# Kernel optimization log

Measured on AMD Instinct MI355X. Metric: run time of the kernel, lower is better.

## Reference

```python
import jax, jax.numpy as jnp
import numpy as np

T, B, H, V, L = 512, 8, 256, 32000, 3
THRESH = 1.0

# Heaviside spike with ATan surrogate gradient (snntorch default, alpha=2)
@jax.custom_vjp
def spike(u):
    return (u > 0).astype(u.dtype)

def _spike_fwd(u):
    return (u > 0).astype(u.dtype), u

def _spike_bwd(u, g):
    return (g / (1.0 + (jnp.pi * u) ** 2),)

spike.defvjp(_spike_fwd, _spike_bwd)


def leaky_scan(cur, beta):
    """mem[t] = beta * mem[t-1] + cur[t]; cur: (T,B,H), beta: (H,). No reset -> associative."""
    def step(mem, c):
        mem = beta * mem + c
        return mem, mem
    _, mems = jax.lax.scan(step, jnp.zeros(cur.shape[1:], cur.dtype), cur)
    return mems  # (T,B,H)


def setup_inputs() -> dict:
    key = jax.random.key(0)
    ks = jax.random.split(key, 10)
    s = 1.0 / np.sqrt(H)
    return {
        "tokens": jax.random.randint(ks[0], (T, B), 0, V),
        "token_emb": jax.random.normal(ks[1], (V, H), dtype=jnp.float32) * 0.02,
        "pos_emb": jax.random.normal(ks[2], (T, H), dtype=jnp.float32) * 0.02,
        "Wq": jax.random.normal(ks[3], (L, H, H), dtype=jnp.float32) * s,
        "bq": jnp.zeros((L, H), dtype=jnp.float32),
        "beta": jax.random.uniform(ks[4], (L, H), minval=0.5, maxval=0.95),
        "Wfc": jax.random.normal(ks[5], (L, H, H), dtype=jnp.float32) * s,
        "bfc": jnp.zeros((L, H), dtype=jnp.float32),
        "Wout": jax.random.normal(ks[6], (H, V), dtype=jnp.float32) * s,
        "bout": jnp.zeros((V,), dtype=jnp.float32),
    }


def reference(tokens, token_emb, pos_emb, Wq, bq, beta, Wfc, bfc, Wout, bout):
    # embed: (T,B,H) + broadcast positional (T,1,H)
    h = token_emb[tokens] + pos_emb[:, None, :]
    for l in range(L):  # small fixed layer count
        cur = jnp.einsum('tbh,hd->tbd', h, Wq[l]) + bq[l]   # q-projection
        mem = leaky_scan(cur, beta[l])                       # leaky integrate, no reset
        spk = spike(mem - THRESH)                            # heaviside spikes
        h = jax.nn.relu(jnp.einsum('tbh,hd->tbd', spk, Wfc[l]) + bfc[l])
    logits = jnp.einsum('tbh,hv->tbv', h, Wout) + bout       # (T,B,V)
    return logits
```

## Files before the change

### kernel.cpp

```cpp
#include <hip/hip_runtime.h>
#include <hip/hip_bf16.h>
#include <cstddef>

constexpr int T_ = 512;
constexpr int B_ = 8;
constexpr int H_ = 256;
constexpr int V_ = 32000;
constexpr int L_ = 3;
constexpr int M_ = T_ * B_;

typedef __attribute__((ext_vector_type(8))) short short8;
typedef __attribute__((ext_vector_type(4))) float floatx4;

__device__ __forceinline__ unsigned short f2bf(float f) {
    unsigned u = __float_as_uint(f);
    u += 0x7fffu + ((u >> 16) & 1u);
    return (unsigned short)(u >> 16);
}

__device__ __forceinline__ void gl_lds16(const void* g, void* l) {
    __builtin_amdgcn_global_load_lds((__attribute__((address_space(1))) void*)g,
                                     (__attribute__((address_space(3))) void*)l,
                                     16, 0, 0);
}

__global__ __launch_bounds__(256) void embed_kernel(
    const int* __restrict__ tokens, const float* __restrict__ temb,
    const float* __restrict__ pemb, unsigned short* __restrict__ hb)
{
    const int idx = blockIdx.x * 256 + threadIdx.x;
    const int h4 = idx & (H_ / 4 - 1);
    const int tb = idx >> 6;
    const int b  = tb & (B_ - 1);
    const int t  = tb >> 3;
    const int tok = tokens[t * B_ + b];
    const float4 e = *(const float4*)&temb[(size_t)tok * H_ + h4 * 4];
    const float4 p = *(const float4*)&pemb[(size_t)t * H_ + h4 * 4];
    ushort4 r;
    r.x = f2bf(e.x + p.x); r.y = f2bf(e.y + p.y);
    r.z = f2bf(e.z + p.z); r.w = f2bf(e.w + p.w);
    *(ushort4*)&hb[(size_t)idx * 4] = r;
}

constexpr int CH_ = 32;
constexpr int NT_ = T_ / CH_;
constexpr int TS_ = B_ * H_;

__global__ __launch_bounds__(256) void scan_local_kernel(
    const float* __restrict__ cur, const float* __restrict__ beta_l,
    float* __restrict__ mloc)
{
    const int c = blockIdx.x, b = blockIdx.y, h = threadIdx.x;
    const float bt = beta_l[h];
    const size_t off = ((size_t)(c * CH_) * B_ + b) * H_ + h;
    const float* p = cur + off;
    float* q = mloc + off;
    float mem = 0.0f;
    #pragma unroll
    for (int tt = 0; tt < CH_; ++tt) {
        mem = fmaf(bt, mem, p[(size_t)tt * TS_]);
        q[(size_t)tt * TS_] = mem;
    }
}

__global__ __launch_bounds__(256) void scan_apply_kernel(
    const float* __restrict__ mloc, const float* __restrict__ beta_l,
    unsigned short* __restrict__ spk)
{
    const int c = blockIdx.x, b = blockIdx.y, h = threadIdx.x;
    const float bt = beta_l[h];
    float b32 = bt;
    #pragma unroll
    for (int i = 0; i < 5; ++i) b32 *= b32;
    float carry = 0.0f;
    for (int j = 0; j < c; ++j)
        carry = fmaf(b32, carry,
                     mloc[((size_t)(j * CH_ + CH_ - 1) * B_ + b) * H_ + h]);
    const size_t off = ((size_t)(c * CH_) * B_ + b) * H_ + h;
    const float* p = mloc + off;
    unsigned short* q = spk + off;
    float pw = bt;
    #pragma unroll
    for (int tt = 0; tt < CH_; ++tt) {
        const float mem = fmaf(pw, carry, p[(size_t)tt * TS_]);
        pw *= bt;
        q[(size_t)tt * TS_] = (mem > 1.0f) ? (unsigned short)0x3F80u
                                           : (unsigned short)0u;
    }
}

__global__ __launch_bounds__(256) void transpose_all_kernel(
    const float* __restrict__ Wq, const float* __restrict__ Wfc,
    const float* __restrict__ Wout,
    unsigned short* __restrict__ WT, unsigned short* __restrict__ WoutT)
{
    __shared__ float t[64][65];
    const int bx = blockIdx.x;
    const float* src; unsigned short* dst;
    int n0, k0, sstride;
    if (bx < 96) {
        const int z = bx >> 4, r = bx & 15;
        src = (z < 3) ? Wq + (size_t)z * H_ * H_
                      : Wfc + (size_t)(z - 3) * H_ * H_;
        dst = WT + (size_t)z * H_ * H_;
        n0 = (r & 3) * 64; k0 = (r >> 2) * 64;
        sstride = H_;
    } else {
        const int nb = bx - 96;
        src = Wout; dst = WoutT;
        n0 = (nb >> 2) * 64; k0 = (nb & 3) * 64;
        sstride = V_;
    }
    const int x = threadIdx.x & 63, y = threadIdx.x >> 6;
    #pragma unroll
    for (int i = 0; i < 16; ++i)
        t[y + 4 * i][x] = src[(size_t)(k0 + y + 4 * i) * sstride + n0 + x];
    __syncthreads();
    #pragma unroll
    for (int i = 0; i < 16; ++i)
        dst[(size_t)(n0 + y + 4 * i) * H_ + k0 + x] = f2bf(t[x][y + 4 * i]);
}


__global__ __launch_bounds__(256, 2) void gemm_mfma_out(
    const unsigned short* __restrict__ A,
    const unsigned short* __restrict__ Bt,
    const float* __restrict__ bias,
    float* __restrict__ C)
{
    constexpr int K = H_, N = V_;
    __shared__ __align__(16) short lA[2][1024][8];
    __shared__ __align__(16) short lB[2][512][8];

    const int tid = threadIdx.x;
    const int lane = tid & 63, wave = tid >> 6;
    const int wm = wave >> 1, wn = wave & 1;
    const int l15 = lane & 15, quad = lane >> 4;
    const int m0 = blockIdx.x * 256;
    const int n0 = blockIdx.y * 128;

    floatx4 acc[8][4] = {};

    auto stage = [&](int buf, int ks) {
        const int k0 = ks * 32;
        #pragma unroll
        for (int j = 0; j < 4; ++j) {
            const int base = (wave * 4 + j) * 64;
            const int s = base + lane;
            const int row = s >> 2;
            const int oct = (s & 3) ^ ((row >> 1) & 3);
            gl_lds16(A + (size_t)(m0 + row) * K + k0 + oct * 8, &lA[buf][base][0]);
        }
        #pragma unroll
        for (int j = 0; j < 2; ++j) {
            const int base = (wave * 2 + j) * 64;
            const int s = base + lane;
            const int row = s >> 2;
            const int oct = (s & 3) ^ ((row >> 1) & 3);
            gl_lds16(Bt + (size_t)(n0 + row) * K + k0 + oct * 8, &lB[buf][base][0]);
        }
    };

    stage(0, 0);
    __syncthreads();

    for (int ks = 0; ks < 8; ++ks) {
        const int cur = ks & 1;
        if (ks < 7) stage(cur ^ 1, ks + 1);
        short8 af[8], bf[4];
        #pragma unroll
        for (int f = 0; f < 8; ++f) {
            const int ra = wm * 128 + f * 16 + l15;
            af[f] = *(const short8*)&lA[cur][ra * 4 + (quad ^ ((ra >> 1) & 3))][0];
        }
        #pragma unroll
        for (int g = 0; g < 4; ++g) {
            const int rb = wn * 64 + g * 16 + l15;
            bf[g] = *(const short8*)&lB[cur][rb * 4 + (quad ^ ((rb >> 1) & 3))][0];
        }
        #pragma unroll
        for (int f = 0; f < 8; ++f)
            #pragma unroll
            for (int g = 0; g < 4; ++g)
                acc[f][g] = __builtin_amdgcn_mfma_f32_16x16x32_bf16(
                    af[f], bf[g], acc[f][g], 0, 0, 0);
        __syncthreads();
    }

    float* scr = (float*)&lA[0][0][0] + (size_t)wave * 1088;
    float bvv[4];
    #pragma unroll
    for (int g = 0; g < 4; ++g)
        bvv[g] = bias[n0 + wn * 64 + g * 16 + l15];

    #pragma unroll
    for (int f = 0; f < 8; ++f) {
        #pragma unroll
        for (int g = 0; g < 4; ++g)
            #pragma unroll
            for (int r = 0; r < 4; ++r)
                scr[(quad * 4 + r) * 68 + g * 16 + l15] = acc[f][g][r] + bvv[g];
        asm volatile("s_waitcnt lgkmcnt(0)" ::: "memory");
        #pragma unroll
        for (int rr = 0; rr < 4; ++rr) {
            const int ml = rr * 4 + quad;
            const floatx4 v = *(const floatx4*)&scr[ml * 68 + l15 * 4];
            const size_t m = (size_t)(m0 + wm * 128 + f * 16 + ml);
            __builtin_nontemporal_store(
                v, (floatx4*)&C[m * (size_t)N + n0 + wn * 64 + l15 * 4]);
        }
        asm volatile("s_waitcnt lgkmcnt(0)" ::: "memory");
    }
}

template <int RELU, int OUT_BF16>
__global__ __launch_bounds__(256) void gemm_mfma_layer(
    const unsigned short* __restrict__ A,
    const unsigned short* __restrict__ Bt,
    const float* __restrict__ bias,
    float* __restrict__ Cf, unsigned short* __restrict__ Cb)
{
    constexpr int K = H_, N = H_;
    __shared__ __align__(16) short lA[512][8];
    __shared__ __align__(16) short lB[512][8];

    const int tid = threadIdx.x;
    const int lane = tid & 63, wave = tid >> 6;
    const int wm = wave >> 1, wn = wave & 1;
    const int l15 = lane & 15, quad = lane >> 4;
    const int m0 = blockIdx.x * 64;
    const int n0 = blockIdx.y * 64;

    floatx4 acc[2][2] = {};

    for (int k0 = 0; k0 < K; k0 += 64) {
        #pragma unroll
        for (int j = 0; j < 2; ++j) {
            const int base = (wave * 2 + j) * 64;
            const int s = base + lane;
            const int row = s >> 3;
            const int oct = (s & 7) ^ (row & 7);
            gl_lds16(A + (size_t)(m0 + row) * K + k0 + oct * 8, &lA[base][0]);
        }
        #pragma unroll
        for (int j = 0; j < 2; ++j) {
            const int base = (wave * 2 + j) * 64;
            const int s = base + lane;
            const int row = s >> 3;
            const int oct = (s & 7) ^ (row & 7);
            gl_lds16(Bt + (size_t)(n0 + row) * K + k0 + oct * 8, &lB[base][0]);
        }
        __syncthreads();

        #pragma unroll
        for (int t = 0; t < 2; ++t) {
            short8 af[2], bf[2];
            #pragma unroll
            for (int f = 0; f < 2; ++f) {
                const int ra = wm * 32 + f * 16 + l15;
                af[f] = *(const short8*)&lA[ra * 8 + ((4 * t + quad) ^ (ra & 7))][0];
            }
            #pragma unroll
            for (int g = 0; g < 2; ++g) {
                const int rb = wn * 32 + g * 16 + l15;
                bf[g] = *(const short8*)&lB[rb * 8 + ((4 * t + quad) ^ (rb & 7))][0];
            }
            #pragma unroll
            for (int f = 0; f < 2; ++f)
                #pragma unroll
                for (int g = 0; g < 2; ++g)
                    acc[f][g] = __builtin_amdgcn_mfma_f32_16x16x32_bf16(
                        af[f], bf[g], acc[f][g], 0, 0, 0);
        }
        __syncthreads();
    }

    #pragma unroll
    for (int g = 0; g < 2; ++g) {
        const int col = n0 + wn * 32 + g * 16 + l15;
        const float bv = bias[col];
        #pragma unroll
        for (int f = 0; f < 2; ++f) {
            const int rbase = m0 + wm * 32 + f * 16 + quad * 4;
            #pragma unroll
            for (int r = 0; r < 4; ++r) {
                float v = acc[f][g][r] + bv;
                if (RELU) v = fmaxf(v, 0.0f);
                if (OUT_BF16)
                    Cb[(size_t)(rbase + r) * N + col] = f2bf(v);
                else
                    Cf[(size_t)(rbase + r) * N + col] = v;
            }
        }
    }
}

extern "C" void kernel_launch(void* const* d_in, const int* in_sizes, int n_in,
                              void* d_out, int out_size, void* d_ws, size_t ws_size,
                              hipStream_t stream)
{
    const int*   tokens = (const int*)  d_in[0];
    const float* temb   = (const float*)d_in[1];
    const float* pemb   = (const float*)d_in[2];
    const float* Wq     = (const float*)d_in[3];
    const float* bq     = (const float*)d_in[4];
    const float* beta   = (const float*)d_in[5];
    const float* Wfc    = (const float*)d_in[6];
    const float* bfc    = (const float*)d_in[7];
    const float* Wout   = (const float*)d_in[8];
    const float* bout   = (const float*)d_in[9];
    float* out = (float*)d_out;

    unsigned short* h_bf  = (unsigned short*)d_ws;
    unsigned short* spk   = h_bf + (size_t)M_ * H_;
    unsigned short* WT    = spk + (size_t)M_ * H_;
    unsigned short* WoutT = WT + (size_t)2 * L_ * H_ * H_;
    float*          cur   = (float*)(WoutT + (size_t)V_ * H_);
    float*          mloc  = cur + (size_t)M_ * H_;

    transpose_all_kernel<<<96 + (V_ / 64) * (H_ / 64), 256, 0, stream>>>(
        Wq, Wfc, Wout, WT, WoutT);

    embed_kernel<<<(M_ * H_ / 4) / 256, 256, 0, stream>>>(tokens, temb, pemb, h_bf);

    for (int l = 0; l < L_; ++l) {
        const unsigned short* WqT  = WT + (size_t)l * H_ * H_;
        const unsigned short* WfcT = WT + (size_t)(L_ + l) * H_ * H_;
        gemm_mfma_layer<0, 0><<<dim3(M_ / 64, H_ / 64), 256, 0, stream>>>(
            h_bf, WqT, bq + (size_t)l * H_, cur, nullptr);
        scan_local_kernel<<<dim3(NT_, B_), 256, 0, stream>>>(
            cur, beta + (size_t)l * H_, mloc);
        scan_apply_kernel<<<dim3(NT_, B_), 256, 0, stream>>>(
            mloc, beta + (size_t)l * H_, spk);
        gemm_mfma_layer<1, 1><<<dim3(M_ / 64, H_ / 64), 256, 0, stream>>>(
            spk, WfcT, bfc + (size_t)l * H_, nullptr, h_bf);
    }

    gemm_mfma_out<<<dim3(M_ / 256, V_ / 128), 256, 0, stream>>>(
        h_bf, WoutT, bout, out);
}
```

Baseline: 661.0 us.

## Fuse two-pass chunked scan into single kernel recomputing prefix per chunk

The two-kernel chunked scan (local scan plus carry/apply) becomes one kernel. Each chunk block sequentially re-scans all earlier timesteps from the raw currents to get its starting membrane, then emits spikes for its own chunk. This drops a launch and the mloc write/read round trip per layer, but adds redundant serial prefix work that grows with chunk index, up to 480 steps for the last chunk. The output GEMM also switches its logits stores from nontemporal to regular stores.

```diff
diff --git a/kernel.cpp b/kernel.cpp
--- a/kernel.cpp
+++ b/kernel.cpp
@@ -46,44 +46,23 @@
 constexpr int NT_ = T_ / CH_;
 constexpr int TS_ = B_ * H_;
 
-__global__ __launch_bounds__(256) void scan_local_kernel(
+__global__ __launch_bounds__(256) void scan_spike_kernel(
     const float* __restrict__ cur, const float* __restrict__ beta_l,
-    float* __restrict__ mloc)
+    unsigned short* __restrict__ spk)
 {
     const int c = blockIdx.x, b = blockIdx.y, h = threadIdx.x;
     const float bt = beta_l[h];
-    const size_t off = ((size_t)(c * CH_) * B_ + b) * H_ + h;
-    const float* p = cur + off;
-    float* q = mloc + off;
+    const float* p = cur + (size_t)b * H_ + h;
     float mem = 0.0f;
+    const int pre = c * CH_;
+    #pragma unroll 8
+    for (int t = 0; t < pre; ++t)
+        mem = fmaf(bt, mem, p[(size_t)t * TS_]);
+    const float* pc = p + (size_t)pre * TS_;
+    unsigned short* q = spk + ((size_t)pre * B_ + b) * H_ + h;
     #pragma unroll
     for (int tt = 0; tt < CH_; ++tt) {
-        mem = fmaf(bt, mem, p[(size_t)tt * TS_]);
-        q[(size_t)tt * TS_] = mem;
-    }
-}
-
-__global__ __launch_bounds__(256) void scan_apply_kernel(
-    const float* __restrict__ mloc, const float* __restrict__ beta_l,
-    unsigned short* __restrict__ spk)
-{
-    const int c = blockIdx.x, b = blockIdx.y, h = threadIdx.x;
-    const float bt = beta_l[h];
-    float b32 = bt;
-    #pragma unroll
-    for (int i = 0; i < 5; ++i) b32 *= b32;
-    float carry = 0.0f;
-    for (int j = 0; j < c; ++j)
-        carry = fmaf(b32, carry,
-                     mloc[((size_t)(j * CH_ + CH_ - 1) * B_ + b) * H_ + h]);
-    const size_t off = ((size_t)(c * CH_) * B_ + b) * H_ + h;
-    const float* p = mloc + off;
-    unsigned short* q = spk + off;
-    float pw = bt;
-    #pragma unroll
-    for (int tt = 0; tt < CH_; ++tt) {
-        const float mem = fmaf(pw, carry, p[(size_t)tt * TS_]);
-        pw *= bt;
+        mem = fmaf(bt, mem, pc[(size_t)tt * TS_]);
         q[(size_t)tt * TS_] = (mem > 1.0f) ? (unsigned short)0x3F80u
                                            : (unsigned short)0u;
     }
@@ -206,8 +185,7 @@
             const int ml = rr * 4 + quad;
             const floatx4 v = *(const floatx4*)&scr[ml * 68 + l15 * 4];
             const size_t m = (size_t)(m0 + wm * 128 + f * 16 + ml);
-            __builtin_nontemporal_store(
-                v, (floatx4*)&C[m * (size_t)N + n0 + wn * 64 + l15 * 4]);
+            *(floatx4*)&C[m * (size_t)N + n0 + wn * 64 + l15 * 4] = v;
         }
         asm volatile("s_waitcnt lgkmcnt(0)" ::: "memory");
     }
@@ -316,7 +294,6 @@
     unsigned short* WT    = spk + (size_t)M_ * H_;
     unsigned short* WoutT = WT + (size_t)2 * L_ * H_ * H_;
     float*          cur   = (float*)(WoutT + (size_t)V_ * H_);
-    float*          mloc  = cur + (size_t)M_ * H_;
 
     transpose_all_kernel<<<96 + (V_ / 64) * (H_ / 64), 256, 0, stream>>>(
         Wq, Wfc, Wout, WT, WoutT);
@@ -328,10 +305,8 @@
         const unsigned short* WfcT = WT + (size_t)(L_ + l) * H_ * H_;
         gemm_mfma_layer<0, 0><<<dim3(M_ / 64, H_ / 64), 256, 0, stream>>>(
             h_bf, WqT, bq + (size_t)l * H_, cur, nullptr);
-        scan_local_kernel<<<dim3(NT_, B_), 256, 0, stream>>>(
-            cur, beta + (size_t)l * H_, mloc);
-        scan_apply_kernel<<<dim3(NT_, B_), 256, 0, stream>>>(
-            mloc, beta + (size_t)l * H_, spk);
+        scan_spike_kernel<<<dim3(NT_, B_), 256, 0, stream>>>(
+            cur, beta + (size_t)l * H_, spk);
         gemm_mfma_layer<1, 1><<<dim3(M_ / 64, H_ / 64), 256, 0, stream>>>(
             spk, WfcT, bfc + (size_t)l * H_, nullptr, h_bf);
     }
```

Measured after the change: 822.8 us. +24.5%, slower.

## Fuse embedding and all layer stages into one cooperative persistent kernel

Applied to the files above, without the earlier changes.

Replaces the embed kernel and the per-layer sequence of GEMM, two scan kernels and second GEMM (13 launches) with one cooperative kernel of 256 blocks that uses grid-wide syncs between phases. This removes launch gaps and kernel boundary overheads in the small, latency-bound middle section. In exchange, half the blocks sit idle during the scan phases, and grid.sync with threadfences adds its own barrier cost.

```diff
diff --git a/kernel.cpp b/kernel.cpp
--- a/kernel.cpp
+++ b/kernel.cpp
@@ -1,6 +1,9 @@
 #include <hip/hip_runtime.h>
 #include <hip/hip_bf16.h>
+#include <hip/hip_cooperative_groups.h>
 #include <cstddef>
+
+namespace cg = cooperative_groups;
 
 constexpr int T_ = 512;
 constexpr int B_ = 8;
@@ -22,71 +25,6 @@
     __builtin_amdgcn_global_load_lds((__attribute__((address_space(1))) void*)g,
                                      (__attribute__((address_space(3))) void*)l,
                                      16, 0, 0);
-}
-
-__global__ __launch_bounds__(256) void embed_kernel(
-    const int* __restrict__ tokens, const float* __restrict__ temb,
-    const float* __restrict__ pemb, unsigned short* __restrict__ hb)
-{
-    const int idx = blockIdx.x * 256 + threadIdx.x;
-    const int h4 = idx & (H_ / 4 - 1);
-    const int tb = idx >> 6;
-    const int b  = tb & (B_ - 1);
-    const int t  = tb >> 3;
-    const int tok = tokens[t * B_ + b];
-    const float4 e = *(const float4*)&temb[(size_t)tok * H_ + h4 * 4];
-    const float4 p = *(const float4*)&pemb[(size_t)t * H_ + h4 * 4];
-    ushort4 r;
-    r.x = f2bf(e.x + p.x); r.y = f2bf(e.y + p.y);
-    r.z = f2bf(e.z + p.z); r.w = f2bf(e.w + p.w);
-    *(ushort4*)&hb[(size_t)idx * 4] = r;
-}
-
-constexpr int CH_ = 32;
-constexpr int NT_ = T_ / CH_;
-constexpr int TS_ = B_ * H_;
-
-__global__ __launch_bounds__(256) void scan_local_kernel(
-    const float* __restrict__ cur, const float* __restrict__ beta_l,
-    float* __restrict__ mloc)
-{
-    const int c = blockIdx.x, b = blockIdx.y, h = threadIdx.x;
-    const float bt = beta_l[h];
-    const size_t off = ((size_t)(c * CH_) * B_ + b) * H_ + h;
-    const float* p = cur + off;
-    float* q = mloc + off;
-    float mem = 0.0f;
-    #pragma unroll
-    for (int tt = 0; tt < CH_; ++tt) {
-        mem = fmaf(bt, mem, p[(size_t)tt * TS_]);
-        q[(size_t)tt * TS_] = mem;
-    }
-}
-
-__global__ __launch_bounds__(256) void scan_apply_kernel(
-    const float* __restrict__ mloc, const float* __restrict__ beta_l,
-    unsigned short* __restrict__ spk)
-{
-    const int c = blockIdx.x, b = blockIdx.y, h = threadIdx.x;
-    const float bt = beta_l[h];
-    float b32 = bt;
-    #pragma unroll
-    for (int i = 0; i < 5; ++i) b32 *= b32;
-    float carry = 0.0f;
-    for (int j = 0; j < c; ++j)
-        carry = fmaf(b32, carry,
-                     mloc[((size_t)(j * CH_ + CH_ - 1) * B_ + b) * H_ + h]);
-    const size_t off = ((size_t)(c * CH_) * B_ + b) * H_ + h;
-    const float* p = mloc + off;
-    unsigned short* q = spk + off;
-    float pw = bt;
-    #pragma unroll
-    for (int tt = 0; tt < CH_; ++tt) {
-        const float mem = fmaf(pw, carry, p[(size_t)tt * TS_]);
-        pw *= bt;
-        q[(size_t)tt * TS_] = (mem > 1.0f) ? (unsigned short)0x3F80u
-                                           : (unsigned short)0u;
-    }
 }
 
 __global__ __launch_bounds__(256) void transpose_all_kernel(
@@ -122,114 +60,23 @@
 }
 
 
-__global__ __launch_bounds__(256, 2) void gemm_mfma_out(
-    const unsigned short* __restrict__ A,
-    const unsigned short* __restrict__ Bt,
-    const float* __restrict__ bias,
-    float* __restrict__ C)
-{
-    constexpr int K = H_, N = V_;
-    __shared__ __align__(16) short lA[2][1024][8];
-    __shared__ __align__(16) short lB[2][512][8];
-
-    const int tid = threadIdx.x;
+constexpr int CH_ = 32;
+constexpr int NT_ = T_ / CH_;
+constexpr int TS_ = B_ * H_;
+
+template <int RELU, int OUT_BF16>
+__device__ __forceinline__ void gemm_layer_phase(
+    const unsigned short* __restrict__ A, const unsigned short* __restrict__ Bt,
+    const float* __restrict__ bias, float* __restrict__ Cf,
+    unsigned short* __restrict__ Cb, short (*lA)[8], short (*lB)[8],
+    int bx, int tid)
+{
+    constexpr int K = H_, N = H_;
     const int lane = tid & 63, wave = tid >> 6;
     const int wm = wave >> 1, wn = wave & 1;
     const int l15 = lane & 15, quad = lane >> 4;
-    const int m0 = blockIdx.x * 256;
-    const int n0 = blockIdx.y * 128;
-
-    floatx4 acc[8][4] = {};
-
-    auto stage = [&](int buf, int ks) {
-        const int k0 = ks * 32;
-        #pragma unroll
-        for (int j = 0; j < 4; ++j) {
-            const int base = (wave * 4 + j) * 64;
-            const int s = base + lane;
-            const int row = s >> 2;
-            const int oct = (s & 3) ^ ((row >> 1) & 3);
-            gl_lds16(A + (size_t)(m0 + row) * K + k0 + oct * 8, &lA[buf][base][0]);
-        }
-        #pragma unroll
-        for (int j = 0; j < 2; ++j) {
-            const int base = (wave * 2 + j) * 64;
-            const int s = base + lane;
-            const int row = s >> 2;
-            const int oct = (s & 3) ^ ((row >> 1) & 3);
-            gl_lds16(Bt + (size_t)(n0 + row) * K + k0 + oct * 8, &lB[buf][base][0]);
-        }
-    };
-
-    stage(0, 0);
-    __syncthreads();
-
-    for (int ks = 0; ks < 8; ++ks) {
-        const int cur = ks & 1;
-        if (ks < 7) stage(cur ^ 1, ks + 1);
-        short8 af[8], bf[4];
-        #pragma unroll
-        for (int f = 0; f < 8; ++f) {
-            const int ra = wm * 128 + f * 16 + l15;
-            af[f] = *(const short8*)&lA[cur][ra * 4 + (quad ^ ((ra >> 1) & 3))][0];
-        }
-        #pragma unroll
-        for (int g = 0; g < 4; ++g) {
-            const int rb = wn * 64 + g * 16 + l15;
-            bf[g] = *(const short8*)&lB[cur][rb * 4 + (quad ^ ((rb >> 1) & 3))][0];
-        }
-        #pragma unroll
-        for (int f = 0; f < 8; ++f)
-            #pragma unroll
-            for (int g = 0; g < 4; ++g)
-                acc[f][g] = __builtin_amdgcn_mfma_f32_16x16x32_bf16(
-                    af[f], bf[g], acc[f][g], 0, 0, 0);
-        __syncthreads();
-    }
-
-    float* scr = (float*)&lA[0][0][0] + (size_t)wave * 1088;
-    float bvv[4];
-    #pragma unroll
-    for (int g = 0; g < 4; ++g)
-        bvv[g] = bias[n0 + wn * 64 + g * 16 + l15];
-
-    #pragma unroll
-    for (int f = 0; f < 8; ++f) {
-        #pragma unroll
-        for (int g = 0; g < 4; ++g)
-            #pragma unroll
-            for (int r = 0; r < 4; ++r)
-                scr[(quad * 4 + r) * 68 + g * 16 + l15] = acc[f][g][r] + bvv[g];
-        asm volatile("s_waitcnt lgkmcnt(0)" ::: "memory");
-        #pragma unroll
-        for (int rr = 0; rr < 4; ++rr) {
-            const int ml = rr * 4 + quad;
-            const floatx4 v = *(const floatx4*)&scr[ml * 68 + l15 * 4];
-            const size_t m = (size_t)(m0 + wm * 128 + f * 16 + ml);
-            __builtin_nontemporal_store(
-                v, (floatx4*)&C[m * (size_t)N + n0 + wn * 64 + l15 * 4]);
-        }
-        asm volatile("s_waitcnt lgkmcnt(0)" ::: "memory");
-    }
-}
-
-template <int RELU, int OUT_BF16>
-__global__ __launch_bounds__(256) void gemm_mfma_layer(
-    const unsigned short* __restrict__ A,
-    const unsigned short* __restrict__ Bt,
-    const float* __restrict__ bias,
-    float* __restrict__ Cf, unsigned short* __restrict__ Cb)
-{
-    constexpr int K = H_, N = H_;
-    __shared__ __align__(16) short lA[512][8];
-    __shared__ __align__(16) short lB[512][8];
-
-    const int tid = threadIdx.x;
-    const int lane = tid & 63, wave = tid >> 6;
-    const int wm = wave >> 1, wn = wave & 1;
-    const int l15 = lane & 15, quad = lane >> 4;
-    const int m0 = blockIdx.x * 64;
-    const int n0 = blockIdx.y * 64;
+    const int m0 = (bx >> 2) * 64;
+    const int n0 = (bx & 3) * 64;
 
     floatx4 acc[2][2] = {};
 
@@ -292,6 +139,189 @@
                     Cf[(size_t)(rbase + r) * N + col] = v;
             }
         }
+    }
+}
+
+__global__ __launch_bounds__(256) void fused_layers_coop(
+    const int* __restrict__ tokens, const float* __restrict__ temb,
+    const float* __restrict__ pemb, const unsigned short* __restrict__ WT,
+    const float* __restrict__ bq, const float* __restrict__ beta,
+    const float* __restrict__ bfc, unsigned short* __restrict__ h_bf,
+    unsigned short* __restrict__ spk, float* __restrict__ cur,
+    float* __restrict__ mloc)
+{
+    __shared__ __align__(16) short lA[512][8];
+    __shared__ __align__(16) short lB[512][8];
+
+    cg::grid_group grid = cg::this_grid();
+    const int bx = blockIdx.x, tid = threadIdx.x;
+
+    #pragma unroll
+    for (int i = 0; i < 4; ++i) {
+        const int idx = (bx + 256 * i) * 256 + tid;
+        const int h4 = idx & (H_ / 4 - 1);
+        const int tb = idx >> 6;
+        const int b  = tb & (B_ - 1);
+        const int t  = tb >> 3;
+        const int tok = tokens[t * B_ + b];
+        const float4 e = *(const float4*)&temb[(size_t)tok * H_ + h4 * 4];
+        const float4 p = *(const float4*)&pemb[(size_t)t * H_ + h4 * 4];
+        ushort4 r;
+        r.x = f2bf(e.x + p.x); r.y = f2bf(e.y + p.y);
+        r.z = f2bf(e.z + p.z); r.w = f2bf(e.w + p.w);
+        *(ushort4*)&h_bf[(size_t)idx * 4] = r;
+    }
+    __threadfence();
+    grid.sync();
+
+    for (int l = 0; l < L_; ++l) {
+        const unsigned short* WqT  = WT + (size_t)l * H_ * H_;
+        const unsigned short* WfcT = WT + (size_t)(L_ + l) * H_ * H_;
+        const float* beta_l = beta + (size_t)l * H_;
+
+        gemm_layer_phase<0, 0>(h_bf, WqT, bq + (size_t)l * H_, cur, nullptr,
+                               lA, lB, bx, tid);
+        __threadfence();
+        grid.sync();
+
+        if (bx < 128) {
+            const int c = bx & 15, b = bx >> 4, h = tid;
+            const float bt = beta_l[h];
+            const size_t off = ((size_t)(c * CH_) * B_ + b) * H_ + h;
+            const float* p = cur + off;
+            float* q = mloc + off;
+            float mem = 0.0f;
+            #pragma unroll
+            for (int tt = 0; tt < CH_; ++tt) {
+                mem = fmaf(bt, mem, p[(size_t)tt * TS_]);
+                q[(size_t)tt * TS_] = mem;
+            }
+        }
+        __threadfence();
+        grid.sync();
+
+        if (bx < 128) {
+            const int c = bx & 15, b = bx >> 4, h = tid;
+            const float bt = beta_l[h];
+            float b32 = bt;
+            #pragma unroll
+            for (int i = 0; i < 5; ++i) b32 *= b32;
+            float carry = 0.0f;
+            for (int j = 0; j < c; ++j)
+                carry = fmaf(b32, carry,
+                             mloc[((size_t)(j * CH_ + CH_ - 1) * B_ + b) * H_ + h]);
+            const size_t off = ((size_t)(c * CH_) * B_ + b) * H_ + h;
+            const float* p = mloc + off;
+            unsigned short* q = spk + off;
+            float pw = bt;
+            #pragma unroll
+            for (int tt = 0; tt < CH_; ++tt) {
+                const float mem = fmaf(pw, carry, p[(size_t)tt * TS_]);
+                pw *= bt;
+                q[(size_t)tt * TS_] = (mem > 1.0f) ? (unsigned short)0x3F80u
+                                                   : (unsigned short)0u;
+            }
+        }
+        __threadfence();
+        grid.sync();
+
+        gemm_layer_phase<1, 1>(spk, WfcT, bfc + (size_t)l * H_, nullptr, h_bf,
+                               lA, lB, bx, tid);
+        if (l < L_ - 1) {
+            __threadfence();
+            grid.sync();
+        }
+    }
+}
+
+__global__ __launch_bounds__(256, 2) void gemm_mfma_out(
+    const unsigned short* __restrict__ A,
+    const unsigned short* __restrict__ Bt,
+    const float* __restrict__ bias,
+    float* __restrict__ C)
+{
+    constexpr int K = H_, N = V_;
+    __shared__ __align__(16) short lA[2][1024][8];
+    __shared__ __align__(16) short lB[2][512][8];
+
+    const int tid = threadIdx.x;
+    const int lane = tid & 63, wave = tid >> 6;
+    const int wm = wave >> 1, wn = wave & 1;
+    const int l15 = lane & 15, quad = lane >> 4;
+    const int m0 = blockIdx.x * 256;
+    const int n0 = blockIdx.y * 128;
+
+    floatx4 acc[8][4] = {};
+
+    auto stage = [&](int buf, int ks) {
+        const int k0 = ks * 32;
+        #pragma unroll
+        for (int j = 0; j < 4; ++j) {
+            const int base = (wave * 4 + j) * 64;
+            const int s = base + lane;
+            const int row = s >> 2;
+            const int oct = (s & 3) ^ ((row >> 1) & 3);
+            gl_lds16(A + (size_t)(m0 + row) * K + k0 + oct * 8, &lA[buf][base][0]);
+        }
+        #pragma unroll
+        for (int j = 0; j < 2; ++j) {
+            const int base = (wave * 2 + j) * 64;
+            const int s = base + lane;
+            const int row = s >> 2;
+            const int oct = (s & 3) ^ ((row >> 1) & 3);
+            gl_lds16(Bt + (size_t)(n0 + row) * K + k0 + oct * 8, &lB[buf][base][0]);
+        }
+    };
+
+    stage(0, 0);
+    __syncthreads();
+
+    for (int ks = 0; ks < 8; ++ks) {
+        const int cur = ks & 1;
+        if (ks < 7) stage(cur ^ 1, ks + 1);
+        short8 af[8], bf[4];
+        #pragma unroll
+        for (int f = 0; f < 8; ++f) {
+            const int ra = wm * 128 + f * 16 + l15;
+            af[f] = *(const short8*)&lA[cur][ra * 4 + (quad ^ ((ra >> 1) & 3))][0];
+        }
+        #pragma unroll
+        for (int g = 0; g < 4; ++g) {
+            const int rb = wn * 64 + g * 16 + l15;
+            bf[g] = *(const short8*)&lB[cur][rb * 4 + (quad ^ ((rb >> 1) & 3))][0];
+        }
+        #pragma unroll
+        for (int f = 0; f < 8; ++f)
+            #pragma unroll
+            for (int g = 0; g < 4; ++g)
+                acc[f][g] = __builtin_amdgcn_mfma_f32_16x16x32_bf16(
+                    af[f], bf[g], acc[f][g], 0, 0, 0);
+        __syncthreads();
+    }
+
+    float* scr = (float*)&lA[0][0][0] + (size_t)wave * 1088;
+    float bvv[4];
+    #pragma unroll
+    for (int g = 0; g < 4; ++g)
+        bvv[g] = bias[n0 + wn * 64 + g * 16 + l15];
+
+    #pragma unroll
+    for (int f = 0; f < 8; ++f) {
+        #pragma unroll
+        for (int g = 0; g < 4; ++g)
+            #pragma unroll
+            for (int r = 0; r < 4; ++r)
+                scr[(quad * 4 + r) * 68 + g * 16 + l15] = acc[f][g][r] + bvv[g];
+        asm volatile("s_waitcnt lgkmcnt(0)" ::: "memory");
+        #pragma unroll
+        for (int rr = 0; rr < 4; ++rr) {
+            const int ml = rr * 4 + quad;
+            const floatx4 v = *(const floatx4*)&scr[ml * 68 + l15 * 4];
+            const size_t m = (size_t)(m0 + wm * 128 + f * 16 + ml);
+            __builtin_nontemporal_store(
+                v, (floatx4*)&C[m * (size_t)N + n0 + wn * 64 + l15 * 4]);
+        }
+        asm volatile("s_waitcnt lgkmcnt(0)" ::: "memory");
     }
 }
 
@@ -321,20 +351,14 @@
     transpose_all_kernel<<<96 + (V_ / 64) * (H_ / 64), 256, 0, stream>>>(
         Wq, Wfc, Wout, WT, WoutT);
 
-    embed_kernel<<<(M_ * H_ / 4) / 256, 256, 0, stream>>>(tokens, temb, pemb, h_bf);
-
-    for (int l = 0; l < L_; ++l) {
-        const unsigned short* WqT  = WT + (size_t)l * H_ * H_;
-        const unsigned short* WfcT = WT + (size_t)(L_ + l) * H_ * H_;
-        gemm_mfma_layer<0, 0><<<dim3(M_ / 64, H_ / 64), 256, 0, stream>>>(
-            h_bf, WqT, bq + (size_t)l * H_, cur, nullptr);
-        scan_local_kernel<<<dim3(NT_, B_), 256, 0, stream>>>(
-            cur, beta + (size_t)l * H_, mloc);
-        scan_apply_kernel<<<dim3(NT_, B_), 256, 0, stream>>>(
-            mloc, beta + (size_t)l * H_, spk);
-        gemm_mfma_layer<1, 1><<<dim3(M_ / 64, H_ / 64), 256, 0, stream>>>(
-            spk, WfcT, bfc + (size_t)l * H_, nullptr, h_bf);
-    }
+    const unsigned short* WTc = WT;
+    void* args[] = {
+        (void*)&tokens, (void*)&temb, (void*)&pemb, (void*)&WTc,
+        (void*)&bq, (void*)&beta, (void*)&bfc,
+        (void*)&h_bf, (void*)&spk, (void*)&cur, (void*)&mloc
+    };
+    hipLaunchCooperativeKernel((const void*)fused_layers_coop,
+                               dim3(256), dim3(256), args, 0, stream);
 
     gemm_mfma_out<<<dim3(M_ / 256, V_ / 128), 256, 0, stream>>>(
         h_bf, WoutT, bout, out);
```

Result: slower. 1.301 ms (+96.9%).

## Fuse q-projection with local scan and scan-apply with fc GEMM

Applied to the files above, without the earlier changes.

Replaces the four per-layer kernels with two. The first computes the q-projection for a 32-timestep chunk and runs the chunk-local leaky scan out of LDS. The second applies the cross-chunk carry, builds spikes directly in LDS, and runs the fc GEMM with ReLU. This removes the fp32 cur buffer, the bf16 spike buffer and two launches per layer. The cost is fewer blocks: 64 with 512 threads for the qproj kernel and 128 for the fc kernel, which means low occupancy and a serial carry loop per thread.

```diff
diff --git a/kernel.cpp b/kernel.cpp
--- a/kernel.cpp
+++ b/kernel.cpp
@@ -40,53 +40,6 @@
     r.x = f2bf(e.x + p.x); r.y = f2bf(e.y + p.y);
     r.z = f2bf(e.z + p.z); r.w = f2bf(e.w + p.w);
     *(ushort4*)&hb[(size_t)idx * 4] = r;
-}
-
-constexpr int CH_ = 32;
-constexpr int NT_ = T_ / CH_;
-constexpr int TS_ = B_ * H_;
-
-__global__ __launch_bounds__(256) void scan_local_kernel(
-    const float* __restrict__ cur, const float* __restrict__ beta_l,
-    float* __restrict__ mloc)
-{
-    const int c = blockIdx.x, b = blockIdx.y, h = threadIdx.x;
-    const float bt = beta_l[h];
-    const size_t off = ((size_t)(c * CH_) * B_ + b) * H_ + h;
-    const float* p = cur + off;
-    float* q = mloc + off;
-    float mem = 0.0f;
-    #pragma unroll
-    for (int tt = 0; tt < CH_; ++tt) {
-        mem = fmaf(bt, mem, p[(size_t)tt * TS_]);
-        q[(size_t)tt * TS_] = mem;
-    }
-}
-
-__global__ __launch_bounds__(256) void scan_apply_kernel(
-    const float* __restrict__ mloc, const float* __restrict__ beta_l,
-    unsigned short* __restrict__ spk)
-{
-    const int c = blockIdx.x, b = blockIdx.y, h = threadIdx.x;
-    const float bt = beta_l[h];
-    float b32 = bt;
-    #pragma unroll
-    for (int i = 0; i < 5; ++i) b32 *= b32;
-    float carry = 0.0f;
-    for (int j = 0; j < c; ++j)
-        carry = fmaf(b32, carry,
-                     mloc[((size_t)(j * CH_ + CH_ - 1) * B_ + b) * H_ + h]);
-    const size_t off = ((size_t)(c * CH_) * B_ + b) * H_ + h;
-    const float* p = mloc + off;
-    unsigned short* q = spk + off;
-    float pw = bt;
-    #pragma unroll
-    for (int tt = 0; tt < CH_; ++tt) {
-        const float mem = fmaf(pw, carry, p[(size_t)tt * TS_]);
-        pw *= bt;
-        q[(size_t)tt * TS_] = (mem > 1.0f) ? (unsigned short)0x3F80u
-                                           : (unsigned short)0u;
-    }
 }
 
 __global__ __launch_bounds__(256) void transpose_all_kernel(
@@ -122,6 +75,215 @@
 }
 
 
+constexpr int CH_ = 32;
+constexpr int NT_ = T_ / CH_;
+
+__global__ __launch_bounds__(512, 1) void qproj_scan_kernel(
+    const unsigned short* __restrict__ A,
+    const unsigned short* __restrict__ Bt,
+    const float* __restrict__ bias,
+    const float* __restrict__ beta_l,
+    float* __restrict__ mloc)
+{
+    constexpr int K = H_;
+    __shared__ __align__(16) char smem[98304];
+    short (*lA)[8] = (short(*)[8])smem;
+    short (*lB)[8] = (short(*)[8])(smem + 65536);
+    float* scr = (float*)smem;
+
+    const int tid = threadIdx.x;
+    const int lane = tid & 63, wave = tid >> 6;
+    const int wm = wave >> 1, wn = wave & 1;
+    const int l15 = lane & 15, quad = lane >> 4;
+    const int c  = blockIdx.x;
+    const int m0 = c * 256;
+    const int n0 = blockIdx.y * 64;
+
+    #pragma unroll
+    for (int j = 0; j < 4; ++j) {
+        const int base = (wave * 4 + j) * 64;
+        const int s = base + lane;
+        const int sub = s >> 9, s2 = s & 511;
+        const int row = s2 >> 3;
+        const int o = (s2 & 7) ^ (row & 7);
+        gl_lds16(Bt + (size_t)(n0 + row) * K + sub * 64 + o * 8, &lB[base][0]);
+    }
+
+    floatx4 acc[4][2] = {};
+
+    #pragma unroll
+    for (int hk = 0; hk < 2; ++hk) {
+        #pragma unroll
+        for (int j = 0; j < 8; ++j) {
+            const int base = (wave * 8 + j) * 64;
+            const int s = base + lane;
+            const int sub = s >> 11, s2 = s & 2047;
+            const int row = s2 >> 3;
+            const int o = (s2 & 7) ^ (row & 7);
+            gl_lds16(A + (size_t)(m0 + row) * K + hk * 128 + sub * 64 + o * 8,
+                     &lA[base][0]);
+        }
+        __syncthreads();
+
+        #pragma unroll
+        for (int ktl = 0; ktl < 4; ++ktl) {
+            const int sub = ktl >> 1, tt = ktl & 1;
+            const int bsub = hk * 2 + sub;
+            short8 af[4], bf[2];
+            #pragma unroll
+            for (int f = 0; f < 4; ++f) {
+                const int ra = wm * 64 + f * 16 + l15;
+                af[f] = *(const short8*)
+                    &lA[sub * 2048 + ra * 8 + ((4 * tt + quad) ^ (ra & 7))][0];
+            }
+            #pragma unroll
+            for (int g = 0; g < 2; ++g) {
+                const int rb = wn * 32 + g * 16 + l15;
+                bf[g] = *(const short8*)
+                    &lB[bsub * 512 + rb * 8 + ((4 * tt + quad) ^ (rb & 7))][0];
+            }
+            #pragma unroll
+            for (int f = 0; f < 4; ++f)
+                #pragma unroll
+                for (int g = 0; g < 2; ++g)
+                    acc[f][g] = __builtin_amdgcn_mfma_f32_16x16x32_bf16(
+                        af[f], bf[g], acc[f][g], 0, 0, 0);
+        }
+        __syncthreads();
+    }
+
+    float bv[2];
+    #pragma unroll
+    for (int g = 0; g < 2; ++g)
+        bv[g] = bias[n0 + wn * 32 + g * 16 + l15];
+    #pragma unroll
+    for (int f = 0; f < 4; ++f)
+        #pragma unroll
+        for (int g = 0; g < 2; ++g)
+            #pragma unroll
+            for (int r = 0; r < 4; ++r)
+                scr[(wm * 64 + f * 16 + quad * 4 + r) * 65 +
+                    wn * 32 + g * 16 + l15] = acc[f][g][r] + bv[g];
+    __syncthreads();
+
+    {
+        const int b = tid >> 6;
+        const int hl = tid & 63;
+        const float bt = beta_l[n0 + hl];
+        float mem = 0.0f;
+        #pragma unroll
+        for (int tt = 0; tt < CH_; ++tt) {
+            mem = fmaf(bt, mem, scr[(tt * 8 + b) * 65 + hl]);
+            mloc[((size_t)(c * CH_ + tt) * B_ + b) * H_ + n0 + hl] = mem;
+        }
+    }
+}
+
+__global__ __launch_bounds__(256) void scan_fc_kernel(
+    const float* __restrict__ mloc,
+    const float* __restrict__ beta_l,
+    const unsigned short* __restrict__ Bt,
+    const float* __restrict__ bias,
+    unsigned short* __restrict__ Cb)
+{
+    constexpr int K = H_, N = H_;
+    __shared__ __align__(16) short lA[4096][8];
+    __shared__ __align__(16) short lB[2048][8];
+
+    const int tid = threadIdx.x;
+    const int lane = tid & 63, wave = tid >> 6;
+    const int wm = wave >> 1, wn = wave & 1;
+    const int l15 = lane & 15, quad = lane >> 4;
+    const int bx = blockIdx.x;
+    const int c = bx >> 1, half = bx & 1;
+    const int m0 = bx * 128;
+    const int n0 = blockIdx.y * 64;
+    const int tw = c * CH_ + half * 16;
+
+    #pragma unroll
+    for (int j = 0; j < 8; ++j) {
+        const int base = (wave * 8 + j) * 64;
+        const int s = base + lane;
+        const int sub = s >> 9, s2 = s & 511;
+        const int row = s2 >> 3;
+        const int o = (s2 & 7) ^ (row & 7);
+        gl_lds16(Bt + (size_t)(n0 + row) * K + sub * 64 + o * 8, &lB[base][0]);
+    }
+
+    {
+        const int b  = tid >> 5;
+        const int h5 = tid & 31;
+        unsigned short* lAu = (unsigned short*)lA;
+        #pragma unroll
+        for (int q = 0; q < 8; ++q) {
+            const int h = q * 32 + h5;
+            const float bt = beta_l[h];
+            float b32 = bt;
+            #pragma unroll
+            for (int i = 0; i < 5; ++i) b32 *= b32;
+            float carry = 0.0f;
+            for (int j = 0; j < c; ++j)
+                carry = fmaf(b32, carry,
+                             mloc[((size_t)(j * CH_ + CH_ - 1) * B_ + b) * H_ + h]);
+            float pw = bt;
+            for (int i = 0; i < half * 16; ++i) pw *= bt;
+            const float* mp = mloc + ((size_t)tw * B_ + b) * H_ + h;
+            #pragma unroll
+            for (int tt = 0; tt < 16; ++tt) {
+                const float mem = fmaf(pw, carry, mp[(size_t)tt * (B_ * H_)]);
+                pw *= bt;
+                const unsigned short sv =
+                    (mem > 1.0f) ? (unsigned short)0x3F80u : (unsigned short)0u;
+                const int row = tt * 8 + b;
+                const int sub = h >> 6, kk = h & 63;
+                const int o = (kk >> 3) ^ (row & 7);
+                lAu[(size_t)(sub * 1024 + row * 8 + o) * 8 + (kk & 7)] = sv;
+            }
+        }
+    }
+    __syncthreads();
+
+    floatx4 acc[4][2] = {};
+    #pragma unroll
+    for (int kt = 0; kt < 8; ++kt) {
+        const int sub = kt >> 1, tt = kt & 1;
+        short8 af[4], bf[2];
+        #pragma unroll
+        for (int f = 0; f < 4; ++f) {
+            const int ra = wm * 64 + f * 16 + l15;
+            af[f] = *(const short8*)
+                &lA[sub * 1024 + ra * 8 + ((4 * tt + quad) ^ (ra & 7))][0];
+        }
+        #pragma unroll
+        for (int g = 0; g < 2; ++g) {
+            const int rb = wn * 32 + g * 16 + l15;
+            bf[g] = *(const short8*)
+                &lB[sub * 512 + rb * 8 + ((4 * tt + quad) ^ (rb & 7))][0];
+        }
+        #pragma unroll
+        for (int f = 0; f < 4; ++f)
+            #pragma unroll
+            for (int g = 0; g < 2; ++g)
+                acc[f][g] = __builtin_amdgcn_mfma_f32_16x16x32_bf16(
+                    af[f], bf[g], acc[f][g], 0, 0, 0);
+    }
+
+    #pragma unroll
+    for (int g = 0; g < 2; ++g) {
+        const int col = n0 + wn * 32 + g * 16 + l15;
+        const float bv = bias[col];
+        #pragma unroll
+        for (int f = 0; f < 4; ++f) {
+            const int rbase = m0 + wm * 64 + f * 16 + quad * 4;
+            #pragma unroll
+            for (int r = 0; r < 4; ++r) {
+                const float v = fmaxf(acc[f][g][r] + bv, 0.0f);
+                Cb[(size_t)(rbase + r) * N + col] = f2bf(v);
+            }
+        }
+    }
+}
+
 __global__ __launch_bounds__(256, 2) void gemm_mfma_out(
     const unsigned short* __restrict__ A,
     const unsigned short* __restrict__ Bt,
@@ -210,88 +372,6 @@
                 v, (floatx4*)&C[m * (size_t)N + n0 + wn * 64 + l15 * 4]);
         }
         asm volatile("s_waitcnt lgkmcnt(0)" ::: "memory");
-    }
-}
-
-template <int RELU, int OUT_BF16>
-__global__ __launch_bounds__(256) void gemm_mfma_layer(
-    const unsigned short* __restrict__ A,
-    const unsigned short* __restrict__ Bt,
-    const float* __restrict__ bias,
-    float* __restrict__ Cf, unsigned short* __restrict__ Cb)
-{
-    constexpr int K = H_, N = H_;
-    __shared__ __align__(16) short lA[512][8];
-    __shared__ __align__(16) short lB[512][8];
-
-    const int tid = threadIdx.x;
-    const int lane = tid & 63, wave = tid >> 6;
-    const int wm = wave >> 1, wn = wave & 1;
-    const int l15 = lane & 15, quad = lane >> 4;
-    const int m0 = blockIdx.x * 64;
-    const int n0 = blockIdx.y * 64;
-
-    floatx4 acc[2][2] = {};
-
-    for (int k0 = 0; k0 < K; k0 += 64) {
-        #pragma unroll
-        for (int j = 0; j < 2; ++j) {
-            const int base = (wave * 2 + j) * 64;
-            const int s = base + lane;
-            const int row = s >> 3;
-            const int oct = (s & 7) ^ (row & 7);
-            gl_lds16(A + (size_t)(m0 + row) * K + k0 + oct * 8, &lA[base][0]);
-        }
-        #pragma unroll
-        for (int j = 0; j < 2; ++j) {
-            const int base = (wave * 2 + j) * 64;
-            const int s = base + lane;
-            const int row = s >> 3;
-            const int oct = (s & 7) ^ (row & 7);
-            gl_lds16(Bt + (size_t)(n0 + row) * K + k0 + oct * 8, &lB[base][0]);
-        }
-        __syncthreads();
-
-        #pragma unroll
-        for (int t = 0; t < 2; ++t) {
-            short8 af[2], bf[2];
-            #pragma unroll
-            for (int f = 0; f < 2; ++f) {
-                const int ra = wm * 32 + f * 16 + l15;
-                af[f] = *(const short8*)&lA[ra * 8 + ((4 * t + quad) ^ (ra & 7))][0];
-            }
-            #pragma unroll
-            for (int g = 0; g < 2; ++g) {
-                const int rb = wn * 32 + g * 16 + l15;
-                bf[g] = *(const short8*)&lB[rb * 8 + ((4 * t + quad) ^ (rb & 7))][0];
-            }
-            #pragma unroll
-            for (int f = 0; f < 2; ++f)
-                #pragma unroll
-                for (int g = 0; g < 2; ++g)
-                    acc[f][g] = __builtin_amdgcn_mfma_f32_16x16x32_bf16(
-                        af[f], bf[g], acc[f][g], 0, 0, 0);
-        }
-        __syncthreads();
-    }
-
-    #pragma unroll
-    for (int g = 0; g < 2; ++g) {
-        const int col = n0 + wn * 32 + g * 16 + l15;
-        const float bv = bias[col];
-        #pragma unroll
-        for (int f = 0; f < 2; ++f) {
-            const int rbase = m0 + wm * 32 + f * 16 + quad * 4;
-            #pragma unroll
-            for (int r = 0; r < 4; ++r) {
-                float v = acc[f][g][r] + bv;
-                if (RELU) v = fmaxf(v, 0.0f);
-                if (OUT_BF16)
-                    Cb[(size_t)(rbase + r) * N + col] = f2bf(v);
-                else
-                    Cf[(size_t)(rbase + r) * N + col] = v;
-            }
-        }
     }
 }
 
@@ -312,11 +392,9 @@
     float* out = (float*)d_out;
 
     unsigned short* h_bf  = (unsigned short*)d_ws;
-    unsigned short* spk   = h_bf + (size_t)M_ * H_;
-    unsigned short* WT    = spk + (size_t)M_ * H_;
+    unsigned short* WT    = h_bf + (size_t)M_ * H_;
     unsigned short* WoutT = WT + (size_t)2 * L_ * H_ * H_;
-    float*          cur   = (float*)(WoutT + (size_t)V_ * H_);
-    float*          mloc  = cur + (size_t)M_ * H_;
+    float*          mloc  = (float*)(WoutT + (size_t)V_ * H_);
 
     transpose_all_kernel<<<96 + (V_ / 64) * (H_ / 64), 256, 0, stream>>>(
         Wq, Wfc, Wout, WT, WoutT);
@@ -326,14 +404,10 @@
     for (int l = 0; l < L_; ++l) {
         const unsigned short* WqT  = WT + (size_t)l * H_ * H_;
         const unsigned short* WfcT = WT + (size_t)(L_ + l) * H_ * H_;
-        gemm_mfma_layer<0, 0><<<dim3(M_ / 64, H_ / 64), 256, 0, stream>>>(
-            h_bf, WqT, bq + (size_t)l * H_, cur, nullptr);
-        scan_local_kernel<<<dim3(NT_, B_), 256, 0, stream>>>(
-            cur, beta + (size_t)l * H_, mloc);
-        scan_apply_kernel<<<dim3(NT_, B_), 256, 0, stream>>>(
-            mloc, beta + (size_t)l * H_, spk);
-        gemm_mfma_layer<1, 1><<<dim3(M_ / 64, H_ / 64), 256, 0, stream>>>(
-            spk, WfcT, bfc + (size_t)l * H_, nullptr, h_bf);
+        qproj_scan_kernel<<<dim3(NT_, 4), 512, 0, stream>>>(
+            h_bf, WqT, bq + (size_t)l * H_, beta + (size_t)l * H_, mloc);
+        scan_fc_kernel<<<dim3(M_ / 128, 4), 256, 0, stream>>>(
+            mloc, beta + (size_t)l * H_, WfcT, bfc + (size_t)l * H_, h_bf);
     }
 
     gemm_mfma_out<<<dim3(M_ / 256, V_ / 128), 256, 0, stream>>>(
```

After: 717.6 us. 1.09x slower.
